# Kernel tuning notes

Measured on AMD Instinct MI355X. Metric: run time of the kernel, lower is better.

The kernel has to match this reference:

```python
import math
import jax, jax.numpy as jnp
import numpy as np

HIDDEN = 1024
HEADS = 16
HEAD_DIM = HIDDEN // HEADS  # 64
SEQ = 4096
PATCH = 4064  # num rotated (patch) tokens; last PATCH positions get RoPE
EPS = 1e-6


def setup_inputs() -> dict:
    key = jax.random.key(0)
    ks = jax.random.split(key, 8)
    return {
        "x": jax.random.normal(ks[0], (1, SEQ, HIDDEN), dtype=jnp.float32),
        "rope_cos": jax.random.uniform(ks[1], (PATCH, HEAD_DIM // 2), dtype=jnp.float32),
        "rope_sin": jax.random.uniform(ks[2], (PATCH, HEAD_DIM // 2), dtype=jnp.float32),
        "wq": jax.random.normal(ks[3], (HIDDEN, HIDDEN), dtype=jnp.float32) / math.sqrt(HIDDEN),
        "wk": jax.random.normal(ks[4], (HIDDEN, HIDDEN), dtype=jnp.float32) / math.sqrt(HIDDEN),
        "wv": jax.random.normal(ks[5], (HIDDEN, HIDDEN), dtype=jnp.float32) / math.sqrt(HIDDEN),
        "wo": jax.random.normal(ks[6], (HIDDEN, HIDDEN), dtype=jnp.float32) / math.sqrt(HIDDEN),
        "q_norm_w": jnp.ones((HEAD_DIM,), dtype=jnp.float32),
        "k_norm_w": jnp.ones((HEAD_DIM,), dtype=jnp.float32),
    }


def _rms_norm(t, w):
    # RMSNorm over the last (head_dim) axis
    return t * jax.lax.rsqrt(jnp.mean(t * t, axis=-1, keepdims=True) + EPS) * w


def _apply_rope(t, cos, sin):
    # t: [b, s, h, d]; rotate only the last PATCH positions, pairwise complex mul
    b, s, h, d = t.shape
    P = cos.shape[0]
    tail = t[:, s - P:].reshape(b, P, h, d // 2, 2)
    x0, x1 = tail[..., 0], tail[..., 1]
    c = cos[None, :, None, :]
    sn = sin[None, :, None, :]
    rot = jnp.stack([x0 * c - x1 * sn, x0 * sn + x1 * c], axis=-1).reshape(b, P, h, d)
    return jnp.concatenate([t[:, : s - P], rot], axis=1)


def reference(x, rope_cos, rope_sin, wq, wk, wv, wo, q_norm_w, k_norm_w):
    b, s, _ = x.shape
    q = (x @ wq.T).reshape(b, s, HEADS, HEAD_DIM)
    k = (x @ wk.T).reshape(b, s, HEADS, HEAD_DIM)
    v = (x @ wv.T).reshape(b, s, HEADS, HEAD_DIM)
    q = _rms_norm(q, q_norm_w)
    k = _rms_norm(k, k_norm_w)
    q = _apply_rope(q, rope_cos, rope_sin)
    k = _apply_rope(k, rope_cos, rope_sin)
    q = q / math.sqrt(HEAD_DIM)
    scores = jnp.einsum('bqhd,bkhd->bhqk', q, k)
    attn = jax.nn.softmax(scores.astype(jnp.float32), axis=-1)
    out = jnp.einsum('bhqk,bkhd->bqhd', attn, v).reshape(b, s, HIDDEN)
    return out @ wo.T
```

## Files before the change

### kernel.cpp

```cpp
#include <hip/hip_runtime.h>
#include <hip/hip_bf16.h>
#include <stdint.h>

#define HIDDEN 1024
#define HEADS 16
#define HEAD_DIM 64
#define SEQ 4096
#define PATCH 4064
#define SKIP 32

typedef __attribute__((ext_vector_type(8))) short bf16x8;
typedef __attribute__((ext_vector_type(4))) float f32x4;
typedef __attribute__((ext_vector_type(2))) float f32x2;
typedef __attribute__((ext_vector_type(16))) float f32x16;

__device__ __forceinline__ float b2f(unsigned short u){
  union{uint32_t i; float f;} c; c.i = ((uint32_t)u)<<16; return c.f;
}
__device__ __forceinline__ unsigned short f2b(float f){
  union{float f; uint32_t i;} c; c.f=f;
  uint32_t r = c.i + 0x7fffu + ((c.i>>16)&1u);
  return (unsigned short)(r>>16);
}
__device__ __forceinline__ uint32_t cvtpk(float a, float b){
  uint32_t r;
  asm("v_cvt_pk_bf16_f32 %0, %1, %2" : "=v"(r) : "v"(a), "v"(b));
  return r;
}

#define GLD16(gp, lp) __builtin_amdgcn_global_load_lds( \
    (const __attribute__((address_space(1))) void*)(gp), \
    (__attribute__((address_space(3))) void*)(lp), 16, 0, 0)

__global__ __launch_bounds__(256) void convert_all(
    const float* __restrict__ x,  const float* __restrict__ wq,
    const float* __restrict__ wk, const float* __restrict__ wv,
    const float* __restrict__ wo,
    unsigned short* __restrict__ xb,  unsigned short* __restrict__ wqb,
    unsigned short* __restrict__ wkb, unsigned short* __restrict__ wvb,
    unsigned short* __restrict__ wob)
{
  size_t u = (size_t)blockIdx.x*256 + threadIdx.x;
  size_t e = u*8;
  const float* src; unsigned short* dst; size_t off;
  if      (e < 4194304ull) { src=x;  dst=xb;  off=e;            }
  else if (e < 5242880ull) { src=wq; dst=wqb; off=e-4194304ull; }
  else if (e < 6291456ull) { src=wk; dst=wkb; off=e-5242880ull; }
  else if (e < 7340032ull) { src=wv; dst=wvb; off=e-6291456ull; }
  else                     { src=wo; dst=wob; off=e-7340032ull; }
  float4 v0 = *(const float4*)(src+off);
  float4 v1 = *(const float4*)(src+off+4);
  union { bf16x8 v; unsigned short h[8]; } o;
  o.h[0]=f2b(v0.x); o.h[1]=f2b(v0.y); o.h[2]=f2b(v0.z); o.h[3]=f2b(v0.w);
  o.h[4]=f2b(v1.x); o.h[5]=f2b(v1.y); o.h[6]=f2b(v1.z); o.h[7]=f2b(v1.w);
  *(bf16x8*)(dst+off) = o.v;
}

__global__ __launch_bounds__(256) void gemm_qkv(
    const unsigned short* __restrict__ A,
    const unsigned short* __restrict__ B0,
    const unsigned short* __restrict__ B1,
    const unsigned short* __restrict__ B2,
    unsigned short* __restrict__ qout, unsigned short* __restrict__ kout,
    unsigned short* __restrict__ vtout,
    const float* __restrict__ rc, const float* __restrict__ rs,
    const float* __restrict__ qw, const float* __restrict__ kw,
    int M, int Nper, int K)
{
  __shared__ unsigned short smem[16896];
  const int tid = threadIdx.x;
  const int w = tid>>6, l = tid&63;
  const int wm = w>>1, wn = w&1;
  const int g = l>>4, lr = l&15;
  const int bm = blockIdx.x;
  int bn = blockIdx.y;
  const int tilesPer = Nper >> 7;
  const int sel = bn / tilesPer;
  bn -= sel*tilesPer;
  const unsigned short* Bsel = (sel==0) ? B0 : ((sel==1) ? B1 : B2);

  const int off0 = w*1024 + l*16;
  const int r0 = off0>>6, c0 = (off0&63)>>1;
  const int off1 = off0 + 4096;
  const int r1 = off1>>6, c1 = (off1&63)>>1;

  const unsigned short* Ab = A    + (size_t)(bm*128)*K;
  const unsigned short* Bb = Bsel + (size_t)(bn*128)*K;

#define STG(db, kt) do { \
    GLD16(Ab + (size_t)r0*K + (kt) + c0, (char*)smem + (db) + off0); \
    GLD16(Ab + (size_t)r1*K + (kt) + c1, (char*)smem + (db) + off1); \
    GLD16(Bb + (size_t)r0*K + (kt) + c0, (char*)smem + (db) + 8192 + off0); \
    GLD16(Bb + (size_t)r1*K + (kt) + c1, (char*)smem + (db) + 8192 + off1); } while(0)

  f32x4 zero = {0.f,0.f,0.f,0.f};
  f32x4 acc[4][4];
  #pragma unroll
  for (int m=0;m<4;m++)
    #pragma unroll
    for (int n=0;n<4;n++) acc[m][n]=zero;

  const int nkt = K >> 5;
  STG(0, 0);
  for (int t = 0; t < nkt; ++t) {
    __syncthreads();
    const int db = (t&1)<<14;
    if (t+1 < nkt) STG(db^16384, (t+1)*32);
    bf16x8 a[4], b[4];
    #pragma unroll
    for (int m=0;m<4;m++)
      a[m] = *(const bf16x8*)((char*)smem + db + (wm*64 + m*16 + lr)*64 + g*16);
    #pragma unroll
    for (int n=0;n<4;n++)
      b[n] = *(const bf16x8*)((char*)smem + db + 8192 + (wn*64 + n*16 + lr)*64 + g*16);
    #pragma unroll
    for (int m=0;m<4;m++)
      #pragma unroll
      for (int n=0;n<4;n++)
        acc[m][n] = __builtin_amdgcn_mfma_f32_16x16x32_bf16(a[m], b[n], acc[m][n], 0,0,0);
  }
#undef STG

  if (sel <= 1) {
    const float* nw = (sel==0) ? qw : kw;
    unsigned short* dst = (sel==0) ? qout : kout;
    const float scl = (sel==0) ? 0.18033688011112042f : 1.0f;
    float wl[4];
    #pragma unroll
    for (int n=0;n<4;n++) wl[n] = nw[n*16+lr];
    const int hglob = bn*2 + wn;
    #pragma unroll
    for (int m=0;m<4;m++){
      const int rowb = bm*128 + wm*64 + m*16 + g*4;
      float rn[4];
      #pragma unroll
      for (int r=0;r<4;r++){
        float ss = 0.f;
        #pragma unroll
        for (int n=0;n<4;n++) ss += acc[m][n][r]*acc[m][n][r];
        ss += __shfl_xor(ss,1); ss += __shfl_xor(ss,2);
        ss += __shfl_xor(ss,4); ss += __shfl_xor(ss,8);
        rn[r] = rsqrtf(ss*(1.f/64.f) + 1e-6f);
      }
      #pragma unroll
      for (int r=0;r<4;r++){
        const int row = rowb + r;
        const int p = row - SKIP;
        #pragma unroll
        for (int n=0;n<4;n++){
          float v = acc[m][n][r]*rn[r]*wl[n];
          float c = 1.f, sn = 0.f;
          if (p >= 0){
            const int d2 = (n*16+lr)>>1;
            c  = rc[p*(HEAD_DIM/2) + d2];
            sn = rs[p*(HEAD_DIM/2) + d2];
          }
          const float partner = __shfl_xor(v, 1);
          const float o2 = (lr&1) ? (partner*sn + v*c) : (v*c - partner*sn);
          dst[(size_t)row*HIDDEN + hglob*64 + n*16 + lr] = f2b(o2*scl);
        }
      }
    }
  } else {
    const int hglob = bn*2 + wn;
    const int sbase = bm*128 + wm*64;
    unsigned short* lchunk = smem + w*4224;
    __syncthreads();
    #pragma unroll
    for (int m=0;m<4;m++)
      #pragma unroll
      for (int n=0;n<4;n++)
        #pragma unroll
        for (int r=0;r<4;r++)
          lchunk[(m*16 + g*4 + r)*66 + n*16 + lr] = f2b(acc[m][n][r]);
    __syncthreads();
    #pragma unroll
    for (int i=0;i<8;i++){
      const int e = i*64 + l;
      const int d = e>>3, sc = (e&7)*8;
      union { bf16x8 v8; unsigned short h8[8]; } o;
      #pragma unroll
      for (int j=0;j<8;j++){
        const int x  = sc + j;
        const int px = (x & ~12) | ((x&4)<<1) | ((x&8)>>1);
        o.h8[j] = lchunk[px*66 + d];
      }
      *(bf16x8*)(vtout + (size_t)(hglob*HEAD_DIM + d)*SEQ + sbase + sc) = o.v8;
    }
  }
}

__global__ __launch_bounds__(256) void gemm_out(
    const unsigned short* __restrict__ A,
    const unsigned short* __restrict__ B,
    float* __restrict__ Cf, int M, int N, int K)
{
  __shared__ unsigned short smem[12288];
  const int tid = threadIdx.x;
  const int w = tid>>6, l = tid&63;
  const int wm = w>>1, wn = w&1;
  const int g = l>>4, lr = l&15;
  const int bm = blockIdx.x;
  const int bn = blockIdx.y;

  const int off0 = w*1024 + l*16;
  const int r0 = off0>>6, c0 = (off0&63)>>1;
  const int off1 = off0 + 4096;
  const int r1 = off1>>6, c1 = (off1&63)>>1;
  const int offB = tid*16;
  const int rB = offB>>6, cB = (offB&63)>>1;

  const unsigned short* Ab = A + (size_t)(bm*128)*K;
  const unsigned short* Bb = B + (size_t)(bn*64)*K;

#define STG(db, kt) do { \
    GLD16(Ab + (size_t)r0*K + (kt) + c0, (char*)smem + (db) + off0); \
    GLD16(Ab + (size_t)r1*K + (kt) + c1, (char*)smem + (db) + off1); \
    GLD16(Bb + (size_t)rB*K + (kt) + cB, (char*)smem + (db) + 8192 + offB); } while(0)

  f32x4 zero = {0.f,0.f,0.f,0.f};
  f32x4 acc[4][2];
  #pragma unroll
  for (int m=0;m<4;m++)
    #pragma unroll
    for (int n=0;n<2;n++) acc[m][n]=zero;

  const int nkt = K >> 5;
  STG(0, 0);
  for (int t = 0; t < nkt; ++t) {
    __syncthreads();
    const int db = (t&1)*12288;
    if (t+1 < nkt) STG(db^12288, (t+1)*32);
    bf16x8 a[4], b[2];
    #pragma unroll
    for (int m=0;m<4;m++)
      a[m] = *(const bf16x8*)((char*)smem + db + (wm*64 + m*16 + lr)*64 + g*16);
    #pragma unroll
    for (int n=0;n<2;n++)
      b[n] = *(const bf16x8*)((char*)smem + db + 8192 + (wn*32 + n*16 + lr)*64 + g*16);
    #pragma unroll
    for (int m=0;m<4;m++)
      #pragma unroll
      for (int n=0;n<2;n++)
        acc[m][n] = __builtin_amdgcn_mfma_f32_16x16x32_bf16(a[m], b[n], acc[m][n], 0,0,0);
  }
#undef STG

  #pragma unroll
  for (int m=0;m<4;m++){
    const int row = bm*128 + wm*64 + m*16 + g*4;
    #pragma unroll
    for (int n=0;n<2;n++){
      const int col = bn*64 + wn*32 + n*16 + lr;
      #pragma unroll
      for (int r=0;r<4;r++)
        Cf[(size_t)(row+r)*N + col] = acc[m][n][r];
    }
  }
}

__device__ __forceinline__ void softmax_pack(f32x16 (&st)[2], f32x2 &lacc, bf16x8 (&pf)[4]){
  float pv[32];
  #pragma unroll
  for (int i=0;i<16;i++){
    pv[i]    = __builtin_amdgcn_exp2f(st[0][i]);
    pv[16+i] = __builtin_amdgcn_exp2f(st[1][i]);
  }
  #pragma unroll
  for (int i=0;i<8;i++){
    f32x2 a; a.x = pv[2*i];    a.y = pv[2*i+1];    lacc += a;
    f32x2 b; b.x = pv[16+2*i]; b.y = pv[16+2*i+1]; lacc += b;
  }
  #pragma unroll
  for (int t2=0; t2<2; t2++)
    #pragma unroll
    for (int e=0; e<2; e++){
      union { uint32_t u4[4]; bf16x8 v8; } pu;
      #pragma unroll
      for (int u=0; u<4; u++)
        pu.u4[u] = cvtpk(pv[t2*16+e*8+2*u], pv[t2*16+e*8+2*u+1]);
      pf[2*t2+e] = pu.v8;
    }
}

__global__ __launch_bounds__(512, 1) void attn_kernel(
    const unsigned short* __restrict__ q, const unsigned short* __restrict__ k,
    const unsigned short* __restrict__ vt, unsigned short* __restrict__ at)
{
  __shared__ unsigned short smem[32768];
  __shared__ float lsm[512];
  const int fid = blockIdx.x + 16*blockIdx.y;
  const int h  = (fid&7)*2 + ((fid>>3)&1);
  const int q0 = (fid>>4)*256;
  const int tid = threadIdx.x;
  const int half = tid>>8;
  const int ht = tid&255;
  const int w = (tid>>6)&3, l = tid&63;
  const int hi = l>>5, lo = l&31;
  const int NT = 32;
  const int tbase = half*NT;
  const int hbase = half*32768;

  const int cA = ht, cB = ht + 256;
  const int rA = cA>>3, rB = cB>>3;
  const int colA = ((cA&7)*16) ^ ((rA&7)<<4);
  const int colB = ((cB&7)*16) ^ ((rB&7)<<4);
  const unsigned short* kA = k  + (size_t)rA*HIDDEN + h*HEAD_DIM + (colA>>1);
  const unsigned short* kB = k  + (size_t)rB*HIDDEN + h*HEAD_DIM + (colB>>1);
  const unsigned short* vA = vt + ((size_t)(h*HEAD_DIM + rA))*SEQ + (colA>>1);
  const unsigned short* vB = vt + ((size_t)(h*HEAD_DIM + rB))*SEQ + (colB>>1);

#define STAGE(b, kOffE, vOffE) do { \
    GLD16(kA + (kOffE), (char*)smem + hbase + (b)*16384 + cA*16); \
    GLD16(kB + (kOffE), (char*)smem + hbase + (b)*16384 + cB*16); \
    GLD16(vA + (vOffE), (char*)smem + hbase + (b)*16384 + 8192 + cA*16); \
    GLD16(vB + (vOffE), (char*)smem + hbase + (b)*16384 + 8192 + cB*16); \
  } while(0)

  const int swz = (lo&7)<<4;
  int colo[4];
  #pragma unroll
  for (int ks=0; ks<4; ks++) colo[ks] = ((2*ks+hi)*16) ^ swz;

  bf16x8 qf0[4], qf1[4];
  {
    const unsigned short* qp = q + (size_t)(q0 + w*64 + lo)*HIDDEN + h*HEAD_DIM;
    #pragma unroll
    for (int ks=0; ks<4; ks++){
      qf0[ks] = *(const bf16x8*)(qp + ks*16 + hi*8);
      qf1[ks] = *(const bf16x8*)(qp + 32*HIDDEN + ks*16 + hi*8);
    }
  }

  f32x16 ot0[2], ot1[2];
  #pragma unroll
  for (int m2=0;m2<2;m2++)
    #pragma unroll
    for (int i=0;i<16;i++){ ot0[m2][i] = 0.f; ot1[m2][i] = 0.f; }
  f32x2 lacc0 = {0.f,0.f}, lacc1 = {0.f,0.f};

  STAGE(0, (size_t)tbase*64*HIDDEN, (size_t)tbase*64);

  for (int t = 0; t < NT; ++t) {
    __syncthreads();
    if (t+1 < NT) {
      const size_t ta = (size_t)(tbase + t + 1);
      STAGE((t+1)&1, ta*64*HIDDEN, ta*64);
    }
    const char* Kb = (const char*)smem + hbase + (t&1)*16384;
    const char* Vb = Kb + 8192;

    f32x16 st0[2], st1[2];
    __builtin_amdgcn_s_setprio(1);
    #pragma unroll
    for (int c=0;c<2;c++){
      #pragma unroll
      for (int i=0;i<16;i++){ st0[c][i] = 0.f; st1[c][i] = 0.f; }
      #pragma unroll
      for (int ks=0; ks<4; ks++){
        bf16x8 a = *(const bf16x8*)(Kb + (32*c+lo)*128 + colo[ks]);
        st0[c] = __builtin_amdgcn_mfma_f32_32x32x16_bf16(a, qf0[ks], st0[c], 0,0,0);
        st1[c] = __builtin_amdgcn_mfma_f32_32x32x16_bf16(a, qf1[ks], st1[c], 0,0,0);
      }
    }
    __builtin_amdgcn_s_setprio(0);

    bf16x8 pf0[4], pf1[4];
    softmax_pack(st0, lacc0, pf0);
    softmax_pack(st1, lacc1, pf1);

    __builtin_amdgcn_s_setprio(1);
    #pragma unroll
    for (int m2=0;m2<2;m2++)
      #pragma unroll
      for (int ks=0; ks<4; ks++){
        bf16x8 a = *(const bf16x8*)(Vb + (32*m2+lo)*128 + colo[ks]);
        ot0[m2] = __builtin_amdgcn_mfma_f32_32x32x16_bf16(a, pf0[ks], ot0[m2], 0,0,0);
        ot1[m2] = __builtin_amdgcn_mfma_f32_32x32x16_bf16(a, pf1[ks], ot1[m2], 0,0,0);
      }
    __builtin_amdgcn_s_setprio(0);
  }

  float ls0 = lacc0.x + lacc0.y;
  ls0 += __shfl_xor(ls0, 32);
  float ls1 = lacc1.x + lacc1.y;
  ls1 += __shfl_xor(ls1, 32);

  __syncthreads();
  if (hi == 0){
    lsm[half*256 + w*64 + lo]      = ls0;
    lsm[half*256 + w*64 + 32 + lo] = ls1;
  }
  #pragma unroll
  for (int m2=0;m2<2;m2++)
    #pragma unroll
    for (int f=0; f<4; f++)
      #pragma unroll
      for (int u=0; u<2; u++){
        const int d = 32*m2 + 8*f + 4*hi + 2*u;
        const uint32_t w0 = cvtpk(ot0[m2][4*f+2*u], ot0[m2][4*f+2*u+1]);
        *(uint32_t*)((char*)smem + hbase + (w*64+lo)*128 + ((d*2) ^ swz)) = w0;
        const uint32_t w1 = cvtpk(ot1[m2][4*f+2*u], ot1[m2][4*f+2*u+1]);
        *(uint32_t*)((char*)smem + hbase + (w*64+32+lo)*128 + ((d*2) ^ swz)) = w1;
      }
  __syncthreads();

  {
    const int ql = tid>>1, xh = tid&1;
    const float li = 1.0f / (lsm[ql] + lsm[256 + ql]);
    #pragma unroll
    for (int i=0;i<4;i++){
      const int cb = xh*64 + i*16;
      const int off = ql*128 + (cb ^ ((ql&7)<<4));
      union { bf16x8 v; unsigned short s[8]; } a, b, o;
      a.v = *(const bf16x8*)((const char*)smem + off);
      b.v = *(const bf16x8*)((const char*)smem + 32768 + off);
      #pragma unroll
      for (int j=0;j<8;j++)
        o.s[j] = f2b((b2f(a.s[j]) + b2f(b.s[j])) * li);
      *(bf16x8*)(at + (size_t)(q0+ql)*HIDDEN + h*HEAD_DIM + (cb>>1)) = o.v;
    }
  }
#undef STAGE
}

extern "C" void kernel_launch(void* const* d_in, const int* in_sizes, int n_in,
                              void* d_out, int out_size, void* d_ws, size_t ws_size,
                              hipStream_t stream)
{
  const float* x  = (const float*)d_in[0];
  const float* rc = (const float*)d_in[1];
  const float* rs = (const float*)d_in[2];
  const float* wq = (const float*)d_in[3];
  const float* wk = (const float*)d_in[4];
  const float* wv = (const float*)d_in[5];
  const float* wo = (const float*)d_in[6];
  const float* qw = (const float*)d_in[7];
  const float* kw = (const float*)d_in[8];
  float* out = (float*)d_out;

  char* ws = (char*)d_ws;
  const size_t MB = 1024*1024;
  unsigned short* xb  = (unsigned short*)(ws + 0);
  unsigned short* wqb = (unsigned short*)(ws + 8*MB);
  unsigned short* wkb = (unsigned short*)(ws + 10*MB);
  unsigned short* wvb = (unsigned short*)(ws + 12*MB);
  unsigned short* wob = (unsigned short*)(ws + 14*MB);
  unsigned short* qkv = (unsigned short*)(ws + 16*MB);
  unsigned short* qb = qkv;
  unsigned short* kb = qkv + (size_t)SEQ*HIDDEN;
  unsigned short* vt = (unsigned short*)(ws + 32*MB);
  unsigned short* at = (unsigned short*)(ws + 40*MB);

  convert_all<<<4096, 256, 0, stream>>>(x, wq, wk, wv, wo, xb, wqb, wkb, wvb, wob);
  gemm_qkv<<<dim3(32,24), 256, 0, stream>>>(
      xb, wqb, wkb, wvb, qb, kb, vt, rc, rs, qw, kw, SEQ, HIDDEN, HIDDEN);
  attn_kernel<<<dim3(16,16), 512, 0, stream>>>(qb, kb, vt, at);
  gemm_out<<<dim3(32,16), 256, 0, stream>>>(at, wob, out, SEQ, HIDDEN, HIDDEN);
}
```

Before: 151.3 us.

## Double attention KV tile to 128 keys per stage and remap GEMM block order

The attention kernel now stages 128 keys of K and V per pipeline step instead of 64, using 128KB of LDS. That halves the number of barrier-synchronised iterations and makes each global load batch larger, and each loaded tile is consumed in two 64-key sub-steps. Both GEMM kernels also remap block IDs so that consecutive blocks interleave across groups of eight, likely to spread work across XCDs or improve L2 reuse. The trade-off is much higher LDS use, which could limit occupancy or run into LDS capacity limits.

```diff
diff --git a/kernel.cpp b/kernel.cpp
--- a/kernel.cpp
+++ b/kernel.cpp
@@ -72,8 +72,10 @@
   const int w = tid>>6, l = tid&63;
   const int wm = w>>1, wn = w&1;
   const int g = l>>4, lr = l&15;
-  const int bm = blockIdx.x;
-  int bn = blockIdx.y;
+  const int orig = blockIdx.x + 32*blockIdx.y;
+  const int wg = (orig&7)*96 + (orig>>3);
+  const int bm = wg & 31;
+  int bn = wg >> 5;
   const int tilesPer = Nper >> 7;
   const int sel = bn / tilesPer;
   bn -= sel*tilesPer;
@@ -200,8 +202,10 @@
   const int w = tid>>6, l = tid&63;
   const int wm = w>>1, wn = w&1;
   const int g = l>>4, lr = l&15;
-  const int bm = blockIdx.x;
-  const int bn = blockIdx.y;
+  const int orig = blockIdx.x + 32*blockIdx.y;
+  const int wg = (orig&7)*64 + (orig>>3);
+  const int bm = wg & 31;
+  const int bn = wg >> 5;
 
   const int off0 = w*1024 + l*16;
   const int r0 = off0>>6, c0 = (off0&63)>>1;
@@ -287,7 +291,7 @@
     const unsigned short* __restrict__ q, const unsigned short* __restrict__ k,
     const unsigned short* __restrict__ vt, unsigned short* __restrict__ at)
 {
-  __shared__ unsigned short smem[32768];
+  __shared__ unsigned short smem[65536];
   __shared__ float lsm[512];
   const int fid = blockIdx.x + 16*blockIdx.y;
   const int h  = (fid&7)*2 + ((fid>>3)&1);
@@ -297,24 +301,31 @@
   const int ht = tid&255;
   const int w = (tid>>6)&3, l = tid&63;
   const int hi = l>>5, lo = l&31;
-  const int NT = 32;
+  const int NT = 16;
   const int tbase = half*NT;
-  const int hbase = half*32768;
-
-  const int cA = ht, cB = ht + 256;
-  const int rA = cA>>3, rB = cB>>3;
-  const int colA = ((cA&7)*16) ^ ((rA&7)<<4);
-  const int colB = ((cB&7)*16) ^ ((rB&7)<<4);
-  const unsigned short* kA = k  + (size_t)rA*HIDDEN + h*HEAD_DIM + (colA>>1);
-  const unsigned short* kB = k  + (size_t)rB*HIDDEN + h*HEAD_DIM + (colB>>1);
-  const unsigned short* vA = vt + ((size_t)(h*HEAD_DIM + rA))*SEQ + (colA>>1);
-  const unsigned short* vB = vt + ((size_t)(h*HEAD_DIM + rB))*SEQ + (colB>>1);
+  const int hbase = half*65536;
+
+  const unsigned short* kPtr[4]; const unsigned short* vPtr[4];
+  #pragma unroll
+  for (int i=0;i<4;i++){
+    const int c = ht + i*256;
+    const int rk = c>>3;
+    const int kcol = ((c&7)*16) ^ ((rk&7)<<4);
+    const int rv = c>>4;
+    const int vcol = (((c&7)*16) ^ ((rv&7)<<4)) + ((c>>3)&1)*128;
+    kPtr[i] = k  + (size_t)rk*HIDDEN + h*HEAD_DIM + (kcol>>1);
+    vPtr[i] = vt + ((size_t)(h*HEAD_DIM + rv))*SEQ + (vcol>>1);
+  }
 
 #define STAGE(b, kOffE, vOffE) do { \
-    GLD16(kA + (kOffE), (char*)smem + hbase + (b)*16384 + cA*16); \
-    GLD16(kB + (kOffE), (char*)smem + hbase + (b)*16384 + cB*16); \
-    GLD16(vA + (vOffE), (char*)smem + hbase + (b)*16384 + 8192 + cA*16); \
-    GLD16(vB + (vOffE), (char*)smem + hbase + (b)*16384 + 8192 + cB*16); \
+    GLD16(kPtr[0] + (kOffE), (char*)smem + hbase + (b)*32768 + (ht      )*16); \
+    GLD16(kPtr[1] + (kOffE), (char*)smem + hbase + (b)*32768 + (ht+ 256 )*16); \
+    GLD16(kPtr[2] + (kOffE), (char*)smem + hbase + (b)*32768 + (ht+ 512 )*16); \
+    GLD16(kPtr[3] + (kOffE), (char*)smem + hbase + (b)*32768 + (ht+ 768 )*16); \
+    GLD16(vPtr[0] + (vOffE), (char*)smem + hbase + (b)*32768 + 16384 + (ht      )*16); \
+    GLD16(vPtr[1] + (vOffE), (char*)smem + hbase + (b)*32768 + 16384 + (ht+ 256 )*16); \
+    GLD16(vPtr[2] + (vOffE), (char*)smem + hbase + (b)*32768 + 16384 + (ht+ 512 )*16); \
+    GLD16(vPtr[3] + (vOffE), (char*)smem + hbase + (b)*32768 + 16384 + (ht+ 768 )*16); \
   } while(0)
 
   const int swz = (lo&7)<<4;
@@ -339,46 +350,51 @@
     for (int i=0;i<16;i++){ ot0[m2][i] = 0.f; ot1[m2][i] = 0.f; }
   f32x2 lacc0 = {0.f,0.f}, lacc1 = {0.f,0.f};
 
-  STAGE(0, (size_t)tbase*64*HIDDEN, (size_t)tbase*64);
+  STAGE(0, (size_t)tbase*128*HIDDEN, (size_t)tbase*128);
 
   for (int t = 0; t < NT; ++t) {
     __syncthreads();
     if (t+1 < NT) {
       const size_t ta = (size_t)(tbase + t + 1);
-      STAGE((t+1)&1, ta*64*HIDDEN, ta*64);
-    }
-    const char* Kb = (const char*)smem + hbase + (t&1)*16384;
-    const char* Vb = Kb + 8192;
-
-    f32x16 st0[2], st1[2];
-    __builtin_amdgcn_s_setprio(1);
-    #pragma unroll
-    for (int c=0;c<2;c++){
-      #pragma unroll
-      for (int i=0;i<16;i++){ st0[c][i] = 0.f; st1[c][i] = 0.f; }
-      #pragma unroll
-      for (int ks=0; ks<4; ks++){
-        bf16x8 a = *(const bf16x8*)(Kb + (32*c+lo)*128 + colo[ks]);
-        st0[c] = __builtin_amdgcn_mfma_f32_32x32x16_bf16(a, qf0[ks], st0[c], 0,0,0);
-        st1[c] = __builtin_amdgcn_mfma_f32_32x32x16_bf16(a, qf1[ks], st1[c], 0,0,0);
+      STAGE((t+1)&1, ta*128*HIDDEN, ta*128);
+    }
+    const char* Kb = (const char*)smem + hbase + (t&1)*32768;
+    const char* Vb = Kb + 16384;
+
+    #pragma unroll
+    for (int sub=0; sub<2; ++sub) {
+      const char* Ks = Kb + sub*8192;
+
+      f32x16 st0[2], st1[2];
+      __builtin_amdgcn_s_setprio(1);
+      #pragma unroll
+      for (int c=0;c<2;c++){
+        #pragma unroll
+        for (int i=0;i<16;i++){ st0[c][i] = 0.f; st1[c][i] = 0.f; }
+        #pragma unroll
+        for (int ks=0; ks<4; ks++){
+          bf16x8 a = *(const bf16x8*)(Ks + (32*c+lo)*128 + colo[ks]);
+          st0[c] = __builtin_amdgcn_mfma_f32_32x32x16_bf16(a, qf0[ks], st0[c], 0,0,0);
+          st1[c] = __builtin_amdgcn_mfma_f32_32x32x16_bf16(a, qf1[ks], st1[c], 0,0,0);
+        }
       }
-    }
-    __builtin_amdgcn_s_setprio(0);
-
-    bf16x8 pf0[4], pf1[4];
-    softmax_pack(st0, lacc0, pf0);
-    softmax_pack(st1, lacc1, pf1);
-
-    __builtin_amdgcn_s_setprio(1);
-    #pragma unroll
-    for (int m2=0;m2<2;m2++)
-      #pragma unroll
-      for (int ks=0; ks<4; ks++){
-        bf16x8 a = *(const bf16x8*)(Vb + (32*m2+lo)*128 + colo[ks]);
-        ot0[m2] = __builtin_amdgcn_mfma_f32_32x32x16_bf16(a, pf0[ks], ot0[m2], 0,0,0);
-        ot1[m2] = __builtin_amdgcn_mfma_f32_32x32x16_bf16(a, pf1[ks], ot1[m2], 0,0,0);
-      }
-    __builtin_amdgcn_s_setprio(0);
+      __builtin_amdgcn_s_setprio(0);
+
+      bf16x8 pf0[4], pf1[4];
+      softmax_pack(st0, lacc0, pf0);
+      softmax_pack(st1, lacc1, pf1);
+
+      __builtin_amdgcn_s_setprio(1);
+      #pragma unroll
+      for (int m2=0;m2<2;m2++)
+        #pragma unroll
+        for (int ks=0; ks<4; ks++){
+          bf16x8 a = *(const bf16x8*)(Vb + (32*m2+lo)*256 + sub*128 + colo[ks]);
+          ot0[m2] = __builtin_amdgcn_mfma_f32_32x32x16_bf16(a, pf0[ks], ot0[m2], 0,0,0);
+          ot1[m2] = __builtin_amdgcn_mfma_f32_32x32x16_bf16(a, pf1[ks], ot1[m2], 0,0,0);
+        }
+      __builtin_amdgcn_s_setprio(0);
+    }
   }
 
   float ls0 = lacc0.x + lacc0.y;
@@ -414,7 +430,7 @@
       const int off = ql*128 + (cb ^ ((ql&7)<<4));
       union { bf16x8 v; unsigned short s[8]; } a, b, o;
       a.v = *(const bf16x8*)((const char*)smem + off);
-      b.v = *(const bf16x8*)((const char*)smem + 32768 + off);
+      b.v = *(const bf16x8*)((const char*)smem + 65536 + off);
       #pragma unroll
       for (int j=0;j<8;j++)
         o.s[j] = f2b((b2f(a.s[j]) + b2f(b.s[j])) * li);
```

Result: slower. 157.2 us (+3.9%).
